# Optimization experiments

Measured on AMD Instinct MI355X. Metric: run time of the kernel, lower is better.

Reference implementation:

```python
import jax, jax.numpy as jnp
import numpy as np


def setup_inputs() -> dict:
    key = jax.random.key(0)
    kq, kk, kv = jax.random.split(key, 3)
    B, S, D = 4, 4096, 64
    q = jax.random.normal(kq, (B, S, D), dtype=jnp.float32)
    k = jax.random.normal(kk, (B, S, D), dtype=jnp.float32)
    v = jax.random.normal(kv, (B, S, D), dtype=jnp.float32)
    return {"q": q, "k": k, "v": v}


def reference(q, k, v):
    # q,k,v: [B,S,D]. Faithful to the torch module:
    #   attn = softmax(q @ k^T / sqrt(D))  -- softmax over full row (NOT pre-masked)
    #   attn = attn.masked_fill(tril==0, 0.0)  -- post-softmax causal zeroing
    #   out  = attn @ v
    S = q.shape[1]
    d = jnp.sqrt(jnp.asarray(q.shape[-1], dtype=q.dtype))
    scores = jnp.einsum("bqd,bkd->bqk", q, k) / d  # [B,S,S]
    attn = jax.nn.softmax(scores, axis=-1)
    # causal tril mask sliced from the registered buffer mask[:S,:S]
    causal = jnp.tril(jnp.ones((S, S), dtype=bool))  # [S,S]
    attn = jnp.where(causal[None, :, :], attn, jnp.asarray(0.0, dtype=attn.dtype))
    out = jnp.einsum("bqk,bkd->bqd", attn, v)  # [B,S,D]
    return out
```

## Files before the change

### kernel.cpp

```cpp
#include <hip/hip_runtime.h>
#include <math.h>


typedef _Float16 f16;
typedef __attribute__((ext_vector_type(8))) _Float16 f16x8;
typedef __attribute__((ext_vector_type(16))) float f32x16;

constexpr int S = 4096, D = 64, TK = 32;
constexpr int B_ = 4;
constexpr int NKT = S / TK;
constexpr int WPB = 4;
constexpr int TPW = NKT / WPB;
constexpr int LDV = 40;
constexpr float QSC = 0.125f * 1.44269504088896340736f;

__global__ __launch_bounds__(256) void prep(
    const float* __restrict__ K, const float* __restrict__ V,
    f16* __restrict__ Kfrag, f16* __restrict__ Vfrag) {
  const int bx = blockIdx.x, tid = threadIdx.x;
  if (bx < B_ * NKT) {
    const float* src = K + (size_t)bx * TK * D;
    const int key = tid >> 3, j = tid & 7;
    float4 f0 = *reinterpret_cast<const float4*>(src + key * D + j * 8);
    float4 f1 = *reinterpret_cast<const float4*>(src + key * D + j * 8 + 4);
    f16x8 h;
    h[0] = (f16)f0.x; h[1] = (f16)f0.y; h[2] = (f16)f0.z; h[3] = (f16)f0.w;
    h[4] = (f16)f1.x; h[5] = (f16)f1.y; h[6] = (f16)f1.z; h[7] = (f16)f1.w;
    const int kc = j >> 1, h2 = j & 1;
    const int lane = key + 32 * h2;
    *reinterpret_cast<f16x8*>(Kfrag + ((size_t)bx * 4 + kc) * 512 + lane * 8) = h;
  } else {
    __shared__ float t32[TK][D + 4];
    const int vb = bx - B_ * NKT;
    const float* src = V + (size_t)vb * TK * D;
    #pragma unroll
    for (int r = 0; r < 2; ++r) {
      int f4 = tid + r * 256;
      int row = f4 >> 4, c4 = (f4 & 15) * 4;
      *reinterpret_cast<float4*>(&t32[row][c4]) =
          *reinterpret_cast<const float4*>(src + row * D + c4);
    }
    __syncthreads();
    const int dn = tid >> 7, kc2 = (tid >> 6) & 1, lane = tid & 63;
    const int l31 = lane & 31, h2 = lane >> 5;
    const int dim = dn * 32 + l31;
    const int k0 = kc2 * 16 + 8 * h2;
    f16x8 h;
    #pragma unroll
    for (int jj = 0; jj < 8; ++jj) h[jj] = (f16)t32[k0 + jj][dim];
    *reinterpret_cast<f16x8*>(
        Vfrag + ((size_t)vb * 4 + dn * 2 + kc2) * 512 + lane * 8) = h;
  }
}

__global__ __launch_bounds__(256, 3)
void attn(const float* __restrict__ Q, const f16* __restrict__ Kfrag,
          const f16* __restrict__ Vfrag, float* __restrict__ O) {
  __shared__ union {
    f16 ps[WPB][32][LDV];
    struct { float nb[2][32][68]; float db[WPB][32]; } r;
  } sm;

  const int i = blockIdx.x;
  const int b = (i & 7) >> 1;
  const int t = ((i >> 3) << 1) | (i & 1);
  const int qb = (t & 1) ? (127 - (t >> 1)) : (t >> 1);
  const int q0 = qb * TK;

  const int tid = threadIdx.x;
  const int w = tid >> 6, lane = tid & 63;
  const int l31 = lane & 31, h2 = lane >> 5;

  const size_t bSD = (size_t)b * S * D;

  f16x8 qh[4], qlo[4];
  {
    const float* qr = Q + bSD + (size_t)(q0 + l31) * D;
    #pragma unroll
    for (int kc = 0; kc < 4; ++kc) {
      float4 f0 = *reinterpret_cast<const float4*>(qr + kc * 16 + 8 * h2);
      float4 f1 = *reinterpret_cast<const float4*>(qr + kc * 16 + 8 * h2 + 4);
      float f[8] = {f0.x, f0.y, f0.z, f0.w, f1.x, f1.y, f1.z, f1.w};
      #pragma unroll
      for (int j = 0; j < 8; ++j) {
        float v = f[j] * QSC;
        f16 hi = (f16)v;
        qh[kc][j] = hi;
        qlo[kc][j] = (f16)(v - (float)hi);
      }
    }
  }

  const f16* kf = Kfrag + (size_t)b * NKT * 2048 + lane * 8;
  const f16* vf = Vfrag + (size_t)b * NKT * 2048 + lane * 8;

  f32x16 on0, on1;
  float ls[16];
  #pragma unroll
  for (int r = 0; r < 16; ++r) { on0[r] = 0.f; on1[r] = 0.f; ls[r] = 0.f; }

  f16x8 bk0, bk1, bk2, bk3;
  {
    const f16* kp = kf + (size_t)w * 2048;
    bk0 = *reinterpret_cast<const f16x8*>(kp);
    bk1 = *reinterpret_cast<const f16x8*>(kp + 512);
    bk2 = *reinterpret_cast<const f16x8*>(kp + 1024);
    bk3 = *reinterpret_cast<const f16x8*>(kp + 1536);
  }

  for (int j = 0; j < TPW; ++j) {
    const int kt = (j << 2) | w;
    const int kbase = kt * TK;
    const bool pv = (kbase <= q0);
    const bool diag = (kbase == q0);

    f16x8 v00, v01, v10, v11;
    if (pv) {
      const f16* vp = vf + (size_t)kt * 2048;
      v00 = *reinterpret_cast<const f16x8*>(vp);
      v01 = *reinterpret_cast<const f16x8*>(vp + 512);
      v10 = *reinterpret_cast<const f16x8*>(vp + 1024);
      v11 = *reinterpret_cast<const f16x8*>(vp + 1536);
    }

    f16x8 kn0, kn1, kn2, kn3;
    if (j + 1 < TPW) {
      const f16* kpn = kf + ((size_t)kt + 4) * 2048;
      kn0 = *reinterpret_cast<const f16x8*>(kpn);
      kn1 = *reinterpret_cast<const f16x8*>(kpn + 512);
      kn2 = *reinterpret_cast<const f16x8*>(kpn + 1024);
      kn3 = *reinterpret_cast<const f16x8*>(kpn + 1536);
    }

    f32x16 acc;
    #pragma unroll
    for (int r = 0; r < 16; ++r) acc[r] = 0.f;
    acc = __builtin_amdgcn_mfma_f32_32x32x16_f16(qlo[0], bk0, acc, 0, 0, 0);
    acc = __builtin_amdgcn_mfma_f32_32x32x16_f16(qh[0],  bk0, acc, 0, 0, 0);
    acc = __builtin_amdgcn_mfma_f32_32x32x16_f16(qlo[1], bk1, acc, 0, 0, 0);
    acc = __builtin_amdgcn_mfma_f32_32x32x16_f16(qh[1],  bk1, acc, 0, 0, 0);
    acc = __builtin_amdgcn_mfma_f32_32x32x16_f16(qlo[2], bk2, acc, 0, 0, 0);
    acc = __builtin_amdgcn_mfma_f32_32x32x16_f16(qh[2],  bk2, acc, 0, 0, 0);
    acc = __builtin_amdgcn_mfma_f32_32x32x16_f16(qlo[3], bk3, acc, 0, 0, 0);
    acc = __builtin_amdgcn_mfma_f32_32x32x16_f16(qh[3],  bk3, acc, 0, 0, 0);

    if (pv) {
      #pragma unroll
      for (int r = 0; r < 16; ++r) {
        float pp = __builtin_amdgcn_exp2f(acc[r]);
        f16 ph = (f16)pp;
        ls[r] += (float)ph;
        const int row = (r & 3) + 8 * (r >> 2) + 4 * h2;
        sm.ps[w][row][l31] = (!diag || l31 <= row) ? ph : (f16)0.f;
      }
    } else {
      #pragma unroll
      for (int r = 0; r < 16; ++r)
        ls[r] += __builtin_amdgcn_exp2f(acc[r]);
    }

    if (pv) {
      asm volatile("s_waitcnt lgkmcnt(0)" ::: "memory");
      f16x8 ap0 = *reinterpret_cast<const f16x8*>(&sm.ps[w][l31][8 * h2]);
      f16x8 ap1 = *reinterpret_cast<const f16x8*>(&sm.ps[w][l31][16 + 8 * h2]);
      on0 = __builtin_amdgcn_mfma_f32_32x32x16_f16(ap0, v00, on0, 0, 0, 0);
      on0 = __builtin_amdgcn_mfma_f32_32x32x16_f16(ap1, v01, on0, 0, 0, 0);
      on1 = __builtin_amdgcn_mfma_f32_32x32x16_f16(ap0, v10, on1, 0, 0, 0);
      on1 = __builtin_amdgcn_mfma_f32_32x32x16_f16(ap1, v11, on1, 0, 0, 0);
    }

    bk0 = kn0; bk1 = kn1; bk2 = kn2; bk3 = kn3;
  }

  #pragma unroll
  for (int r = 0; r < 16; ++r) {
    float v = ls[r];
    #pragma unroll
    for (int x = 1; x <= 16; x <<= 1) v += __shfl_xor(v, x);
    ls[r] = v;
  }
  __syncthreads();
  if (l31 == 0) {
    #pragma unroll
    for (int r = 0; r < 16; ++r)
      sm.r.db[w][(r & 3) + 8 * (r >> 2) + 4 * h2] = ls[r];
  }
  if (w < 2) {
    #pragma unroll
    for (int r = 0; r < 16; ++r) {
      const int row = (r & 3) + 8 * (r >> 2) + 4 * h2;
      sm.r.nb[w][row][l31]      = on0[r];
      sm.r.nb[w][row][32 + l31] = on1[r];
    }
  }
  __syncthreads();
  if (w >= 2) {
    #pragma unroll
    for (int r = 0; r < 16; ++r) {
      const int row = (r & 3) + 8 * (r >> 2) + 4 * h2;
      sm.r.nb[w - 2][row][l31]      += on0[r];
      sm.r.nb[w - 2][row][32 + l31] += on1[r];
    }
  }
  __syncthreads();

  #pragma unroll
  for (int it = 0; it < 2; ++it) {
    const int i4 = tid + it * 256;
    const int row = i4 >> 4, c4 = (i4 & 15) * 4;
    float dsum = 0.f;
    #pragma unroll
    for (int ww = 0; ww < WPB; ++ww) dsum += sm.r.db[ww][row];
    const float inv = 1.f / dsum;
    float4 a0 = *reinterpret_cast<const float4*>(&sm.r.nb[0][row][c4]);
    float4 a1 = *reinterpret_cast<const float4*>(&sm.r.nb[1][row][c4]);
    float4 o;
    o.x = (a0.x + a1.x) * inv;
    o.y = (a0.y + a1.y) * inv;
    o.z = (a0.z + a1.z) * inv;
    o.w = (a0.w + a1.w) * inv;
    *reinterpret_cast<float4*>(O + bSD + (size_t)(q0 + row) * D + c4) = o;
  }
}

extern "C" void kernel_launch(void* const* d_in, const int* in_sizes, int n_in,
                              void* d_out, int out_size, void* d_ws, size_t ws_size,
                              hipStream_t stream) {
  const float* q = (const float*)d_in[0];
  const float* k = (const float*)d_in[1];
  const float* v = (const float*)d_in[2];
  float* o = (float*)d_out;

  f16* Kfrag = (f16*)d_ws;
  f16* Vfrag = Kfrag + (size_t)B_ * S * D;

  prep<<<dim3(2 * B_ * NKT), dim3(256), 0, stream>>>(k, v, Kfrag, Vfrag);
  attn<<<dim3(512), dim3(256), 0, stream>>>(q, Kfrag, Vfrag, o);
}
```

Measured before the change: 97.88 us.

## Compute transposed scores and pass P to PV MFMA via permlane swap instead of LDS

Swaps the MFMA operand order so the score tile comes out transposed. Each lane then holds values for one query row, so the per-row denominator becomes a lane-local sum plus one cross-half shuffle instead of a 5-step butterfly per row. The probability tile is repacked into the A-operand layout with v_permlane32_swap rather than a round trip through shared memory, which removes LDS writes and reads and the lgkmcnt wait from the inner loop. This relies on gfx950-specific permlane semantics and a correct register fragment mapping.

```diff
diff --git a/kernel.cpp b/kernel.cpp
--- a/kernel.cpp
+++ b/kernel.cpp
@@ -5,13 +5,13 @@
 typedef _Float16 f16;
 typedef __attribute__((ext_vector_type(8))) _Float16 f16x8;
 typedef __attribute__((ext_vector_type(16))) float f32x16;
+typedef __attribute__((ext_vector_type(4))) unsigned int uint4x;
 
 constexpr int S = 4096, D = 64, TK = 32;
 constexpr int B_ = 4;
 constexpr int NKT = S / TK;
 constexpr int WPB = 4;
 constexpr int TPW = NKT / WPB;
-constexpr int LDV = 40;
 constexpr float QSC = 0.125f * 1.44269504088896340736f;
 
 __global__ __launch_bounds__(256) void prep(
@@ -56,10 +56,7 @@
 __global__ __launch_bounds__(256, 3)
 void attn(const float* __restrict__ Q, const f16* __restrict__ Kfrag,
           const f16* __restrict__ Vfrag, float* __restrict__ O) {
-  __shared__ union {
-    f16 ps[WPB][32][LDV];
-    struct { float nb[2][32][68]; float db[WPB][32]; } r;
-  } sm;
+  __shared__ struct { float nb[2][32][68]; float db[WPB][32]; } sm;
 
   const int i = blockIdx.x;
   const int b = (i & 7) >> 1;
@@ -95,9 +92,11 @@
   const f16* vf = Vfrag + (size_t)b * NKT * 2048 + lane * 8;
 
   f32x16 on0, on1;
-  float ls[16];
+  float dv[4];
   #pragma unroll
-  for (int r = 0; r < 16; ++r) { on0[r] = 0.f; on1[r] = 0.f; ls[r] = 0.f; }
+  for (int r = 0; r < 16; ++r) { on0[r] = 0.f; on1[r] = 0.f; }
+  #pragma unroll
+  for (int r = 0; r < 4; ++r) dv[r] = 0.f;
 
   f16x8 bk0, bk1, bk2, bk3;
   {
@@ -135,62 +134,66 @@
     f32x16 acc;
     #pragma unroll
     for (int r = 0; r < 16; ++r) acc[r] = 0.f;
-    acc = __builtin_amdgcn_mfma_f32_32x32x16_f16(qlo[0], bk0, acc, 0, 0, 0);
-    acc = __builtin_amdgcn_mfma_f32_32x32x16_f16(qh[0],  bk0, acc, 0, 0, 0);
-    acc = __builtin_amdgcn_mfma_f32_32x32x16_f16(qlo[1], bk1, acc, 0, 0, 0);
-    acc = __builtin_amdgcn_mfma_f32_32x32x16_f16(qh[1],  bk1, acc, 0, 0, 0);
-    acc = __builtin_amdgcn_mfma_f32_32x32x16_f16(qlo[2], bk2, acc, 0, 0, 0);
-    acc = __builtin_amdgcn_mfma_f32_32x32x16_f16(qh[2],  bk2, acc, 0, 0, 0);
-    acc = __builtin_amdgcn_mfma_f32_32x32x16_f16(qlo[3], bk3, acc, 0, 0, 0);
-    acc = __builtin_amdgcn_mfma_f32_32x32x16_f16(qh[3],  bk3, acc, 0, 0, 0);
+    acc = __builtin_amdgcn_mfma_f32_32x32x16_f16(bk0, qlo[0], acc, 0, 0, 0);
+    acc = __builtin_amdgcn_mfma_f32_32x32x16_f16(bk0, qh[0],  acc, 0, 0, 0);
+    acc = __builtin_amdgcn_mfma_f32_32x32x16_f16(bk1, qlo[1], acc, 0, 0, 0);
+    acc = __builtin_amdgcn_mfma_f32_32x32x16_f16(bk1, qh[1],  acc, 0, 0, 0);
+    acc = __builtin_amdgcn_mfma_f32_32x32x16_f16(bk2, qlo[2], acc, 0, 0, 0);
+    acc = __builtin_amdgcn_mfma_f32_32x32x16_f16(bk2, qh[2],  acc, 0, 0, 0);
+    acc = __builtin_amdgcn_mfma_f32_32x32x16_f16(bk3, qlo[3], acc, 0, 0, 0);
+    acc = __builtin_amdgcn_mfma_f32_32x32x16_f16(bk3, qh[3],  acc, 0, 0, 0);
 
     if (pv) {
+      unsigned pw[8];
+      const int kb4 = 4 * h2;
       #pragma unroll
-      for (int r = 0; r < 16; ++r) {
-        float pp = __builtin_amdgcn_exp2f(acc[r]);
-        f16 ph = (f16)pp;
-        ls[r] += (float)ph;
-        const int row = (r & 3) + 8 * (r >> 2) + 4 * h2;
-        sm.ps[w][row][l31] = (!diag || l31 <= row) ? ph : (f16)0.f;
+      for (int i2 = 0; i2 < 8; ++i2) {
+        const int ra = 2 * i2, rb = ra + 1;
+        float pa = __builtin_amdgcn_exp2f(acc[ra]);
+        float pb = __builtin_amdgcn_exp2f(acc[rb]);
+        f16 ha = (f16)pa, hb = (f16)pb;
+        dv[i2 & 3] += (float)ha + (float)hb;
+        unsigned short ba = __builtin_bit_cast(unsigned short, ha);
+        unsigned short bb = __builtin_bit_cast(unsigned short, hb);
+        if (diag) {
+          const int kra = (ra & 3) + 8 * (ra >> 2) + kb4;
+          const int krb = (rb & 3) + 8 * (rb >> 2) + kb4;
+          ba = (kra <= l31) ? ba : (unsigned short)0;
+          bb = (krb <= l31) ? bb : (unsigned short)0;
+        }
+        pw[i2] = (unsigned)ba | ((unsigned)bb << 16);
       }
-    } else {
-      #pragma unroll
-      for (int r = 0; r < 16; ++r)
-        ls[r] += __builtin_amdgcn_exp2f(acc[r]);
-    }
-
-    if (pv) {
-      asm volatile("s_waitcnt lgkmcnt(0)" ::: "memory");
-      f16x8 ap0 = *reinterpret_cast<const f16x8*>(&sm.ps[w][l31][8 * h2]);
-      f16x8 ap1 = *reinterpret_cast<const f16x8*>(&sm.ps[w][l31][16 + 8 * h2]);
+      asm("v_permlane32_swap_b32 %0, %1" : "+v"(pw[0]), "+v"(pw[2]));
+      asm("v_permlane32_swap_b32 %0, %1" : "+v"(pw[1]), "+v"(pw[3]));
+      asm("v_permlane32_swap_b32 %0, %1" : "+v"(pw[4]), "+v"(pw[6]));
+      asm("v_permlane32_swap_b32 %0, %1" : "+v"(pw[5]), "+v"(pw[7]));
+      uint4x u0 = {pw[0], pw[1], pw[2], pw[3]};
+      uint4x u1 = {pw[4], pw[5], pw[6], pw[7]};
+      f16x8 ap0 = __builtin_bit_cast(f16x8, u0);
+      f16x8 ap1 = __builtin_bit_cast(f16x8, u1);
+
       on0 = __builtin_amdgcn_mfma_f32_32x32x16_f16(ap0, v00, on0, 0, 0, 0);
       on0 = __builtin_amdgcn_mfma_f32_32x32x16_f16(ap1, v01, on0, 0, 0, 0);
       on1 = __builtin_amdgcn_mfma_f32_32x32x16_f16(ap0, v10, on1, 0, 0, 0);
       on1 = __builtin_amdgcn_mfma_f32_32x32x16_f16(ap1, v11, on1, 0, 0, 0);
+    } else {
+      #pragma unroll
+      for (int r = 0; r < 16; ++r) dv[r & 3] += __builtin_amdgcn_exp2f(acc[r]);
     }
 
     bk0 = kn0; bk1 = kn1; bk2 = kn2; bk3 = kn3;
   }
 
-  #pragma unroll
-  for (int r = 0; r < 16; ++r) {
-    float v = ls[r];
-    #pragma unroll
-    for (int x = 1; x <= 16; x <<= 1) v += __shfl_xor(v, x);
-    ls[r] = v;
-  }
-  __syncthreads();
-  if (l31 == 0) {
-    #pragma unroll
-    for (int r = 0; r < 16; ++r)
-      sm.r.db[w][(r & 3) + 8 * (r >> 2) + 4 * h2] = ls[r];
-  }
+  float den = dv[0] + dv[1] + dv[2] + dv[3];
+  den += __shfl_xor(den, 32);
+  if (h2 == 0) sm.db[w][l31] = den;
+
   if (w < 2) {
     #pragma unroll
     for (int r = 0; r < 16; ++r) {
       const int row = (r & 3) + 8 * (r >> 2) + 4 * h2;
-      sm.r.nb[w][row][l31]      = on0[r];
-      sm.r.nb[w][row][32 + l31] = on1[r];
+      sm.nb[w][row][l31]      = on0[r];
+      sm.nb[w][row][32 + l31] = on1[r];
     }
   }
   __syncthreads();
@@ -198,8 +201,8 @@
     #pragma unroll
     for (int r = 0; r < 16; ++r) {
       const int row = (r & 3) + 8 * (r >> 2) + 4 * h2;
-      sm.r.nb[w - 2][row][l31]      += on0[r];
-      sm.r.nb[w - 2][row][32 + l31] += on1[r];
+      sm.nb[w - 2][row][l31]      += on0[r];
+      sm.nb[w - 2][row][32 + l31] += on1[r];
     }
   }
   __syncthreads();
@@ -210,10 +213,10 @@
     const int row = i4 >> 4, c4 = (i4 & 15) * 4;
     float dsum = 0.f;
     #pragma unroll
-    for (int ww = 0; ww < WPB; ++ww) dsum += sm.r.db[ww][row];
+    for (int ww = 0; ww < WPB; ++ww) dsum += sm.db[ww][row];
     const float inv = 1.f / dsum;
-    float4 a0 = *reinterpret_cast<const float4*>(&sm.r.nb[0][row][c4]);
-    float4 a1 = *reinterpret_cast<const float4*>(&sm.r.nb[1][row][c4]);
+    float4 a0 = *reinterpret_cast<const float4*>(&sm.nb[0][row][c4]);
+    float4 a1 = *reinterpret_cast<const float4*>(&sm.nb[1][row][c4]);
     float4 o;
     o.x = (a0.x + a1.x) * inv;
     o.y = (a0.y + a1.y) * inv;
```

Result: faster. 94.22 us (-3.7%).
